# Optimization experiments

Measured on AMD Instinct MI355X. Metric: run time of the kernel, lower is better.

Reference implementation:

```python
import jax, jax.numpy as jnp
import numpy as np

K = 10  # hardcoded in the module
F = 3 + 3 * K + 3 * K + K + 3  # 76-dim per-point feature


def setup_inputs() -> dict:
    key = jax.random.key(0)
    k0, k1, k2, k3, k4 = jax.random.split(key, 5)
    B, N = 4, 8192
    input_cloud = jax.random.normal(k0, (B, N, 3), dtype=jnp.float32)
    # Single shared MLP (76 -> 64 -> 3); the original instantiates a fresh
    # randomly-initialized MLP per point, which a fused kernel replaces with
    # shared weights.
    W1 = jax.random.normal(k1, (F, 64), dtype=jnp.float32) * 0.1
    b1 = jax.random.normal(k2, (64,), dtype=jnp.float32) * 0.01
    W2 = jax.random.normal(k3, (64, 3), dtype=jnp.float32) * 0.1
    b2 = jax.random.normal(k4, (3,), dtype=jnp.float32) * 0.01
    return {"input_cloud": input_cloud, "W1": W1, "b1": b1, "W2": W2, "b2": b2}


def _knn_indices(cloud):
    # squared pairwise distances (same ordering as cdist), topk smallest
    sq = jnp.sum(cloud * cloud, axis=-1)  # [B,N]
    d2 = sq[:, :, None] + sq[:, None, :] - 2.0 * jnp.einsum("bnd,bmd->bnm", cloud, cloud)
    _, idx = jax.lax.top_k(-d2, K + 1)  # [B,N,K+1], smallest first (self at 0)
    return idx[:, :, 1:]  # drop self -> [B,N,K]


def reference(input_cloud, W1, b1, W2, b2):
    B, N, _ = input_cloud.shape
    knn_idx = _knn_indices(input_cloud)  # [B,N,K] int32

    # gather neighbors: [B,N,K,3]
    neighbors = jnp.take_along_axis(input_cloud[:, None, :, :],
                                    knn_idx[:, :, :, None], axis=2)
    center = input_cloud  # [B,N,3]
    rel = neighbors - center[:, :, None, :]           # [B,N,K,3]
    dists = jnp.sqrt(jnp.sum(rel * rel, axis=-1))     # [B,N,K]

    # per-point 3x3 covariance of the K neighbors (unbiased, like torch.cov)
    mean = jnp.mean(neighbors, axis=2, keepdims=True)  # [B,N,1,3]
    cen = neighbors - mean
    cov = jnp.einsum("bnki,bnkj->bnij", cen, cen) / (K - 1)  # [B,N,3,3]

    eig = jnp.linalg.eigvalsh(cov)          # ascending [B,N,3]
    l1, l2, l3 = eig[..., 2], eig[..., 1], eig[..., 0]  # descending order
    linearity = (l1 - l2) / l1
    planarity = (l2 - l3) / l1
    scattering = l3 / l1
    geom = jnp.stack([linearity, planarity, scattering], axis=-1)  # [B,N,3]

    feats = jnp.concatenate(
        [center,
         neighbors.reshape(B, N, 3 * K),
         rel.reshape(B, N, 3 * K),
         dists,
         geom], axis=-1)  # [B,N,76]

    h = jax.nn.relu(jnp.einsum("bnf,fh->bnh", feats, W1) + b1)
    out = jax.nn.relu(jnp.einsum("bnh,ho->bno", h, W2) + b2)  # [B,N,3]
    return out
```

## Files before the change

### kernel.cpp

```cpp
#include <hip/hip_runtime.h>
#include <math.h>

#define KNN    10
#define NPTS   8192
#define HID    64
#define NF     76
#define Q      16
#define CAP    64
#define F32_INF __uint_as_float(0x7F800000u)

__device__ __forceinline__ float rl(float v, int lane) {
    return __int_as_float(__builtin_amdgcn_readlane(__float_as_int(v), lane));
}

__global__ __launch_bounds__(256) void prep_kernel(const float* __restrict__ cloud,
                                                   float4* __restrict__ pts4) {
    const int i = blockIdx.x * 256 + threadIdx.x;
    const float x = cloud[i * 3 + 0];
    const float y = cloud[i * 3 + 1];
    const float z = cloud[i * 3 + 2];
    pts4[i] = make_float4(x, y, z, fmaf(z, z, fmaf(y, y, x * x)));
}

__global__ __launch_bounds__(256) void knn_kernel(const float4* __restrict__ pts4,
                                                  unsigned short* __restrict__ knn_idx) {
    __shared__ unsigned long long coll[CAP][65];
    __shared__ float pk[4][Q][17];
    __shared__ int   cnt[64];

    const int t    = threadIdx.x;
    const int w    = t >> 6;
    const int lane = t & 63;
    const int bx   = blockIdx.x;
    const int b    = bx >> 7;
    const int n_base = (bx & 127) * 64 + w * Q;
    const int lq_base = w * Q;

    const float4* pb = pts4 + b * NPTS;

    if (lane < Q) cnt[lq_base + lane] = 0;

    float qxs[Q], qys[Q], qzs[Q], qss[Q];
#pragma unroll
    for (int qq = 0; qq < Q; ++qq) {
        const float4 qv = pb[n_base + qq];
        qxs[qq] = qv.x; qys[qq] = qv.y; qzs[qq] = qv.z; qss[qq] = qv.w;
    }

    float vmin[Q];
#pragma unroll
    for (int qq = 0; qq < Q; ++qq) vmin[qq] = F32_INF;

    float4 cp = pb[lane];
    for (int ti = 0; ti < NPTS / 64; ++ti) {
        const float4 np = (ti < NPTS / 64 - 1) ? pb[(ti + 1) * 64 + lane] : cp;
#pragma unroll
        for (int qq = 0; qq < Q; ++qq) {
            const float dot = fmaf(cp.z, qzs[qq], fmaf(cp.y, qys[qq], cp.x * qxs[qq]));
            const float v = fmaf(-2.0f, dot, cp.w);
            vmin[qq] = fminf(vmin[qq], v);
        }
        cp = np;
    }

#pragma unroll
    for (int qq = 0; qq < Q; ++qq) {
        float v = vmin[qq];
        v = fminf(v, __shfl_xor(v, 32, 64));
        v = fminf(v, __shfl_xor(v, 16, 64));
        if (lane < 16) pk[w][qq][lane] = v;
    }

    float taum_v;
    {
        float md[KNN + 1];
#pragma unroll
        for (int s = 0; s <= KNN; ++s) md[s] = F32_INF;
        const int qsel = lane & 15;
#pragma unroll
        for (int cc = 0; cc < 16; ++cc) {
            float d = pk[w][qsel][cc];
#pragma unroll
            for (int u = 0; u <= KNN; ++u) {
                const float lo = fminf(md[u], d);
                d = fmaxf(md[u], d);
                md[u] = lo;
            }
        }
        taum_v = md[KNN] + 1e-3f;
    }
    float taum[Q];
#pragma unroll
    for (int qq = 0; qq < Q; ++qq) taum[qq] = rl(taum_v, qq);

    float4 cp2 = pb[lane];
    int vj_rel = lane - n_base;
    for (int ti = 0; ti < NPTS / 64; ++ti) {
        const float4 np = (ti < NPTS / 64 - 1) ? pb[(ti + 1) * 64 + lane] : cp2;
#pragma unroll
        for (int qq = 0; qq < Q; ++qq) {
            const float dot = fmaf(cp2.z, qzs[qq], fmaf(cp2.y, qys[qq], cp2.x * qxs[qq]));
            const float v = fmaf(-2.0f, dot, cp2.w);
            if (__builtin_expect(v <= taum[qq] && vj_rel != qq, 0)) {
                const float d2 = fmaf(-2.0f, dot, qss[qq] + cp2.w);
                const unsigned int fb = __float_as_uint(d2);
                const unsigned int m =
                    fb ^ ((unsigned int)((int)fb >> 31) | 0x80000000u);
                const int j = vj_rel + n_base;
                const unsigned long long key =
                    ((unsigned long long)m << 13) | (unsigned long long)(unsigned)j;
                const int slot = atomicAdd(&cnt[lq_base + qq], 1);
                if (slot < CAP) coll[slot][lq_base + qq] = key;
            }
        }
        cp2 = np; vj_rel += 64;
    }
    __syncthreads();

    if (t < 64) {
        const int m = cnt[t];
        int mc = m;
#pragma unroll
        for (int off = 1; off < 64; off <<= 1)
            mc = max(mc, __shfl_xor(mc, off, 64));
        mc = __builtin_amdgcn_readfirstlane(mc);

        const int n = (bx & 127) * 64 + t;

        unsigned long long md[KNN];
#pragma unroll
        for (int s = 0; s < KNN; ++s) md[s] = ~0ULL;

        if (mc <= CAP) {
            for (int cc = 0; cc < mc; ++cc) {
                unsigned long long key = (cc < m) ? coll[cc][t] : ~0ULL;
#pragma unroll
                for (int u = 0; u < KNN; ++u) {
                    const bool lt = key < md[u];
                    const unsigned long long lo = lt ? key : md[u];
                    key = lt ? md[u] : key;
                    md[u] = lo;
                }
            }
        } else {
            const float4 qv = pb[n];
            for (int j = 0; j < NPTS; ++j) {
                const float4 p = pb[j];
                const float dot = fmaf(p.z, qv.z, fmaf(p.y, qv.y, p.x * qv.x));
                const float d2 = fmaf(-2.0f, dot, qv.w + p.w);
                const unsigned int fb = __float_as_uint(d2);
                const unsigned int mm =
                    fb ^ ((unsigned int)((int)fb >> 31) | 0x80000000u);
                unsigned long long key =
                    ((unsigned long long)mm << 13) | (unsigned long long)j;
                key = (j == n) ? ~0ULL : key;
#pragma unroll
                for (int u = 0; u < KNN; ++u) {
                    const bool lt = key < md[u];
                    const unsigned long long lo = lt ? key : md[u];
                    key = lt ? md[u] : key;
                    md[u] = lo;
                }
            }
        }

        unsigned short* outp = knn_idx + ((size_t)b * NPTS + n) * KNN;
#pragma unroll
        for (int s = 0; s < KNN; ++s)
            outp[s] = (unsigned short)(md[s] & 8191u);
    }
}

__global__ __launch_bounds__(256) void feat_mlp_kernel(const float4* __restrict__ pts4,
                                                       const float* __restrict__ W1,
                                                       const float* __restrict__ b1,
                                                       const float* __restrict__ W2,
                                                       const float* __restrict__ b2,
                                                       const unsigned short* __restrict__ knn_idx,
                                                       float* __restrict__ out) {
    __shared__ float w1s[NF * 68];
    __shared__ float b1s[HID];
    __shared__ float w2s[HID * 3];
    __shared__ float b2s[3];
    __shared__ float fs[64][NF + 1];

    const int t = threadIdx.x;
    for (int idx = t; idx < NF * HID; idx += 256)
        w1s[(idx >> 6) * 68 + (idx & 63)] = W1[idx];
    if (t < HID) b1s[t] = b1[t];
    if (t < HID * 3) w2s[t] = W2[t];
    if (t < 3) b2s[t] = b2[t];

    const int pl   = t >> 2;
    const int subh = t & 1;
    const int subf = (t >> 1) & 1;
    const int gid = blockIdx.x * 64 + pl;
    const int b = gid >> 13;
    const int n = gid & (NPTS - 1);
    const float4* pb = pts4 + b * NPTS;

    if ((t & 3) == 0) {
        const float4 cq = pb[n];
        const float cx = cq.x, cy = cq.y, cz = cq.z;

        float nx[KNN], ny[KNN], nz[KNN];
        const unsigned short* ki = knn_idx + (size_t)gid * KNN;
#pragma unroll
        for (int k = 0; k < KNN; ++k) {
            const int j = ki[k];
            const float4 p = pb[j];
            nx[k] = p.x; ny[k] = p.y; nz[k] = p.z;
        }

        float* fr = fs[pl];
        fr[0] = cx; fr[1] = cy; fr[2] = cz;
#pragma unroll
        for (int k = 0; k < KNN; ++k) {
            fr[3 + 3 * k + 0] = nx[k];
            fr[3 + 3 * k + 1] = ny[k];
            fr[3 + 3 * k + 2] = nz[k];
        }
#pragma unroll
        for (int k = 0; k < KNN; ++k) {
            fr[33 + 3 * k + 0] = nx[k] - cx;
            fr[33 + 3 * k + 1] = ny[k] - cy;
            fr[33 + 3 * k + 2] = nz[k] - cz;
        }
#pragma unroll
        for (int k = 0; k < KNN; ++k) {
            const float rx = nx[k] - cx, ry = ny[k] - cy, rz = nz[k] - cz;
            fr[63 + k] = sqrtf(fmaf(rz, rz, fmaf(ry, ry, rx * rx)));
        }

        float mx = 0.f, my = 0.f, mz = 0.f;
#pragma unroll
        for (int k = 0; k < KNN; ++k) { mx += nx[k]; my += ny[k]; mz += nz[k]; }
        mx *= (1.0f / KNN); my *= (1.0f / KNN); mz *= (1.0f / KNN);
        float c00 = 0.f, c01 = 0.f, c02 = 0.f, c11 = 0.f, c12 = 0.f, c22 = 0.f;
#pragma unroll
        for (int k = 0; k < KNN; ++k) {
            const float ex = nx[k] - mx, ey = ny[k] - my, ez = nz[k] - mz;
            c00 = fmaf(ex, ex, c00); c01 = fmaf(ex, ey, c01); c02 = fmaf(ex, ez, c02);
            c11 = fmaf(ey, ey, c11); c12 = fmaf(ey, ez, c12); c22 = fmaf(ez, ez, c22);
        }
        const float sc = 1.0f / (KNN - 1);
        c00 *= sc; c01 *= sc; c02 *= sc; c11 *= sc; c12 *= sc; c22 *= sc;

        const double a00 = c00, a01 = c01, a02 = c02, a11 = c11, a12 = c12, a22 = c22;
        const double qd = (a00 + a11 + a22) / 3.0;
        const double p1 = a01 * a01 + a02 * a02 + a12 * a12;
        const double d00 = a00 - qd, d11 = a11 - qd, d22 = a22 - qd;
        const double p2 = d00 * d00 + d11 * d11 + d22 * d22 + 2.0 * p1;
        double l1, l2, l3;
        if (p2 < 1e-300) {
            l1 = l2 = l3 = qd;
        } else {
            const double p = sqrt(p2 / 6.0);
            const double inv = 1.0 / p;
            const double e00 = d00 * inv, e11 = d11 * inv, e22 = d22 * inv;
            const double e01 = a01 * inv, e02 = a02 * inv, e12 = a12 * inv;
            double detB = e00 * (e11 * e22 - e12 * e12)
                        - e01 * (e01 * e22 - e12 * e02)
                        + e02 * (e01 * e12 - e11 * e02);
            double r = 0.5 * detB;
            r = fmin(1.0, fmax(-1.0, r));
            const double phi = acos(r) / 3.0;
            l1 = qd + 2.0 * p * cos(phi);
            l3 = qd + 2.0 * p * cos(phi + 2.0943951023931953);
            l2 = 3.0 * qd - l1 - l3;
        }
        fr[73] = (float)((l1 - l2) / l1);
        fr[74] = (float)((l2 - l3) / l1);
        fr[75] = (float)(l3 / l1);
    }

    __syncthreads();

    const float* fr = fs[pl];
    const int f0 = subf * 38;

    float h[32];
#pragma unroll
    for (int j = 0; j < 32; ++j) h[j] = (subf == 0) ? b1s[subh * 32 + j] : 0.0f;

#pragma unroll 2
    for (int ff = 0; ff < 38; ++ff) {
        const int f = f0 + ff;
        const float v = fr[f];
        const float4* w4 = reinterpret_cast<const float4*>(w1s + f * 68 + subh * 32);
#pragma unroll
        for (int j4 = 0; j4 < 8; ++j4) {
            const float4 w = w4[j4];
            h[4 * j4 + 0] = fmaf(v, w.x, h[4 * j4 + 0]);
            h[4 * j4 + 1] = fmaf(v, w.y, h[4 * j4 + 1]);
            h[4 * j4 + 2] = fmaf(v, w.z, h[4 * j4 + 2]);
            h[4 * j4 + 3] = fmaf(v, w.w, h[4 * j4 + 3]);
        }
    }

#pragma unroll
    for (int j = 0; j < 32; ++j) h[j] += __shfl_xor(h[j], 2, 64);

    float o0 = 0.f, o1 = 0.f, o2 = 0.f;
#pragma unroll
    for (int j = 0; j < 32; ++j) {
        const float r = fmaxf(h[j], 0.0f);
        const int jj = subh * 32 + j;
        o0 = fmaf(r, w2s[jj * 3 + 0], o0);
        o1 = fmaf(r, w2s[jj * 3 + 1], o1);
        o2 = fmaf(r, w2s[jj * 3 + 2], o2);
    }
    o0 += __shfl_xor(o0, 1, 64);
    o1 += __shfl_xor(o1, 1, 64);
    o2 += __shfl_xor(o2, 1, 64);

    if ((t & 3) == 0) {
        float* op = out + (size_t)gid * 3;
        op[0] = fmaxf(o0 + b2s[0], 0.0f);
        op[1] = fmaxf(o1 + b2s[1], 0.0f);
        op[2] = fmaxf(o2 + b2s[2], 0.0f);
    }
}

extern "C" void kernel_launch(void* const* d_in, const int* in_sizes, int n_in,
                              void* d_out, int out_size, void* d_ws, size_t ws_size,
                              hipStream_t stream) {
    const float* cloud = (const float*)d_in[0];
    const float* W1    = (const float*)d_in[1];
    const float* b1    = (const float*)d_in[2];
    const float* W2    = (const float*)d_in[3];
    const float* b2    = (const float*)d_in[4];
    float* out = (float*)d_out;

    float4* pts4 = (float4*)d_ws;
    unsigned short* knn = (unsigned short*)((char*)d_ws + 4 * NPTS * 16);

    prep_kernel<<<dim3(128), dim3(256), 0, stream>>>(cloud, pts4);
    knn_kernel<<<dim3(512), dim3(256), 0, stream>>>(pts4, knn);
    feat_mlp_kernel<<<dim3(512), dim3(256), 0, stream>>>(pts4, W1, b1, W2, b2, knn, out);
}
```

Measured before the change: 207.3 us.

## Split KNN candidate scan across four waves per query group; use float eigen solve

The KNN kernel now runs 1024 threads per block, so four waves share each 16-query group and each scans a quarter of the candidate points. This cuts the serial scan length per wave and adds parallelism, at the cost of extra block-level barriers and a cross-wave threshold merge through shared memory. Separately, the 3x3 eigenvalue solve in the feature kernel moves from double to float with fast cosine, which removes the slow FP64 transcendentals but gives up some accuracy on ill-conditioned covariances.

```diff
diff --git a/kernel.cpp b/kernel.cpp
--- a/kernel.cpp
+++ b/kernel.cpp
@@ -22,23 +22,27 @@
     pts4[i] = make_float4(x, y, z, fmaf(z, z, fmaf(y, y, x * x)));
 }
 
-__global__ __launch_bounds__(256) void knn_kernel(const float4* __restrict__ pts4,
-                                                  unsigned short* __restrict__ knn_idx) {
+__global__ __launch_bounds__(1024) void knn_kernel(const float4* __restrict__ pts4,
+                                                   unsigned short* __restrict__ knn_idx) {
     __shared__ unsigned long long coll[CAP][65];
-    __shared__ float pk[4][Q][17];
+    __shared__ float pk[16][Q][17];
+    __shared__ float tau_s[64];
     __shared__ int   cnt[64];
 
     const int t    = threadIdx.x;
     const int w    = t >> 6;
     const int lane = t & 63;
+    const int g    = w >> 2;
+    const int h    = w & 3;
     const int bx   = blockIdx.x;
     const int b    = bx >> 7;
-    const int n_base = (bx & 127) * 64 + w * Q;
-    const int lq_base = w * Q;
+    const int n_base = (bx & 127) * 64 + g * Q;
+    const int lq_base = g * Q;
+    const int cb0 = h * (NPTS / 4);
 
     const float4* pb = pts4 + b * NPTS;
 
-    if (lane < Q) cnt[lq_base + lane] = 0;
+    if (t < 64) cnt[t] = 0;
 
     float qxs[Q], qys[Q], qzs[Q], qss[Q];
 #pragma unroll
@@ -51,9 +55,9 @@
 #pragma unroll
     for (int qq = 0; qq < Q; ++qq) vmin[qq] = F32_INF;
 
-    float4 cp = pb[lane];
-    for (int ti = 0; ti < NPTS / 64; ++ti) {
-        const float4 np = (ti < NPTS / 64 - 1) ? pb[(ti + 1) * 64 + lane] : cp;
+    float4 cp = pb[cb0 + lane];
+    for (int ti = 0; ti < NPTS / 4 / 64; ++ti) {
+        const float4 np = (ti < NPTS / 4 / 64 - 1) ? pb[cb0 + (ti + 1) * 64 + lane] : cp;
 #pragma unroll
         for (int qq = 0; qq < Q; ++qq) {
             const float dot = fmaf(cp.z, qzs[qq], fmaf(cp.y, qys[qq], cp.x * qxs[qq]));
@@ -70,16 +74,16 @@
         v = fminf(v, __shfl_xor(v, 16, 64));
         if (lane < 16) pk[w][qq][lane] = v;
     }
-
-    float taum_v;
-    {
+    __syncthreads();
+
+    if (h == 0) {
         float md[KNN + 1];
 #pragma unroll
         for (int s = 0; s <= KNN; ++s) md[s] = F32_INF;
         const int qsel = lane & 15;
 #pragma unroll
-        for (int cc = 0; cc < 16; ++cc) {
-            float d = pk[w][qsel][cc];
+        for (int cc = 0; cc < 64; ++cc) {
+            float d = pk[g * 4 + (cc >> 4)][qsel][cc & 15];
 #pragma unroll
             for (int u = 0; u <= KNN; ++u) {
                 const float lo = fminf(md[u], d);
@@ -87,16 +91,21 @@
                 md[u] = lo;
             }
         }
-        taum_v = md[KNN] + 1e-3f;
-    }
+        if (lane < 16) tau_s[lq_base + lane] = md[KNN] + 1e-3f;
+    }
+    __syncthreads();
+
     float taum[Q];
-#pragma unroll
-    for (int qq = 0; qq < Q; ++qq) taum[qq] = rl(taum_v, qq);
-
-    float4 cp2 = pb[lane];
-    int vj_rel = lane - n_base;
-    for (int ti = 0; ti < NPTS / 64; ++ti) {
-        const float4 np = (ti < NPTS / 64 - 1) ? pb[(ti + 1) * 64 + lane] : cp2;
+    {
+        const float tv = tau_s[lq_base + (lane & 15)];
+#pragma unroll
+        for (int qq = 0; qq < Q; ++qq) taum[qq] = rl(tv, qq);
+    }
+
+    float4 cp2 = pb[cb0 + lane];
+    int vj_rel = cb0 + lane - n_base;
+    for (int ti = 0; ti < NPTS / 4 / 64; ++ti) {
+        const float4 np = (ti < NPTS / 4 / 64 - 1) ? pb[cb0 + (ti + 1) * 64 + lane] : cp2;
 #pragma unroll
         for (int qq = 0; qq < Q; ++qq) {
             const float dot = fmaf(cp2.z, qzs[qq], fmaf(cp2.y, qys[qq], cp2.x * qxs[qq]));
@@ -246,32 +255,31 @@
         const float sc = 1.0f / (KNN - 1);
         c00 *= sc; c01 *= sc; c02 *= sc; c11 *= sc; c12 *= sc; c22 *= sc;
 
-        const double a00 = c00, a01 = c01, a02 = c02, a11 = c11, a12 = c12, a22 = c22;
-        const double qd = (a00 + a11 + a22) / 3.0;
-        const double p1 = a01 * a01 + a02 * a02 + a12 * a12;
-        const double d00 = a00 - qd, d11 = a11 - qd, d22 = a22 - qd;
-        const double p2 = d00 * d00 + d11 * d11 + d22 * d22 + 2.0 * p1;
-        double l1, l2, l3;
-        if (p2 < 1e-300) {
+        const float qd = (c00 + c11 + c22) * (1.0f / 3.0f);
+        const float pp1 = c01 * c01 + c02 * c02 + c12 * c12;
+        const float d00 = c00 - qd, d11 = c11 - qd, d22 = c22 - qd;
+        const float p2 = d00 * d00 + d11 * d11 + d22 * d22 + 2.0f * pp1;
+        float l1, l2, l3;
+        if (p2 < 1e-30f) {
             l1 = l2 = l3 = qd;
         } else {
-            const double p = sqrt(p2 / 6.0);
-            const double inv = 1.0 / p;
-            const double e00 = d00 * inv, e11 = d11 * inv, e22 = d22 * inv;
-            const double e01 = a01 * inv, e02 = a02 * inv, e12 = a12 * inv;
-            double detB = e00 * (e11 * e22 - e12 * e12)
-                        - e01 * (e01 * e22 - e12 * e02)
-                        + e02 * (e01 * e12 - e11 * e02);
-            double r = 0.5 * detB;
-            r = fmin(1.0, fmax(-1.0, r));
-            const double phi = acos(r) / 3.0;
-            l1 = qd + 2.0 * p * cos(phi);
-            l3 = qd + 2.0 * p * cos(phi + 2.0943951023931953);
-            l2 = 3.0 * qd - l1 - l3;
-        }
-        fr[73] = (float)((l1 - l2) / l1);
-        fr[74] = (float)((l2 - l3) / l1);
-        fr[75] = (float)(l3 / l1);
+            const float p = sqrtf(p2 * (1.0f / 6.0f));
+            const float inv = 1.0f / p;
+            const float e00 = d00 * inv, e11 = d11 * inv, e22 = d22 * inv;
+            const float e01 = c01 * inv, e02 = c02 * inv, e12 = c12 * inv;
+            float detB = e00 * (e11 * e22 - e12 * e12)
+                       - e01 * (e01 * e22 - e12 * e02)
+                       + e02 * (e01 * e12 - e11 * e02);
+            float r = 0.5f * detB;
+            r = fminf(1.0f, fmaxf(-1.0f, r));
+            const float phi = acosf(r) * (1.0f / 3.0f);
+            l1 = qd + 2.0f * p * __cosf(phi);
+            l3 = qd + 2.0f * p * __cosf(phi + 2.0943951023931953f);
+            l2 = 3.0f * qd - l1 - l3;
+        }
+        fr[73] = (l1 - l2) / l1;
+        fr[74] = (l2 - l3) / l1;
+        fr[75] = l3 / l1;
     }
 
     __syncthreads();
@@ -336,6 +344,6 @@
     unsigned short* knn = (unsigned short*)((char*)d_ws + 4 * NPTS * 16);
 
     prep_kernel<<<dim3(128), dim3(256), 0, stream>>>(cloud, pts4);
-    knn_kernel<<<dim3(512), dim3(256), 0, stream>>>(pts4, knn);
+    knn_kernel<<<dim3(512), dim3(1024), 0, stream>>>(pts4, knn);
     feat_mlp_kernel<<<dim3(512), dim3(256), 0, stream>>>(pts4, W1, b1, W2, b2, knn, out);
 }
```

New measurement: 187.7 us. 1.1x faster.
